# Performance work log

Hardware: AMD Instinct MI355X
Metric: run time of the kernel (lower is better)

The kernel has to match this reference:

```python
import jax, jax.numpy as jnp
import numpy as np

B, N, L = 512, 64, 64
D = 256          # item_embed_size / hidden_size
H = 256          # linear_hidden_size
V = 100000       # item_size
STEP = 1


def _p(key, shape, std=0.0625):
    return jax.random.uniform(key, shape, jnp.float32, -std, std)


def setup_inputs() -> dict:
    key = jax.random.key(0)
    ks = jax.random.split(key, 32)
    inp = {
        "alias_inputs": jax.random.randint(ks[0], (B, L), 0, N),
        "A": jax.random.uniform(ks[1], (B, N, 2 * N), jnp.float32),
        "items": jax.random.randint(ks[2], (B, N), 0, V),
        "mask": jnp.ones((B, L), jnp.int32),
        # parameters (stored as [in, out]; torch Linear applies x @ W.T + b)
        "emb": _p(ks[3], (V, D)),
        "W_ein": _p(ks[4], (D, D)), "b_ein": _p(ks[5], (D,)),
        "W_eout": _p(ks[6], (D, D)), "b_eout": _p(ks[7], (D,)),
        "b_iah": _p(ks[8], (D,)), "b_oah": _p(ks[9], (D,)),
        "W_i": _p(ks[10], (2 * D, 3 * D)), "b_i": _p(ks[11], (3 * D,)),
        "W_h": _p(ks[12], (D, 3 * D)), "b_h": _p(ks[13], (3 * D,)),
        "W1": _p(ks[14], (D, D)), "b1": _p(ks[15], (D,)),
        "W2": _p(ks[16], (D, D)), "b2": _p(ks[17], (D,)),
        "W3": _p(ks[18], (D, 1)),
        "Wn1": _p(ks[19], (2 * D, H)), "bn1": _p(ks[20], (H,)),
        "Wn2": _p(ks[21], (H, D)), "bn2": _p(ks[22], (D,)),
    }
    return inp


def reference(alias_inputs, A, items, mask,
              emb, W_ein, b_ein, W_eout, b_eout, b_iah, b_oah,
              W_i, b_i, W_h, b_h, W1, b1, W2, b2, W3, Wn1, bn1, Wn2, bn2):
    n = A.shape[1]
    hidden = emb[items]  # [B, N, D] (dropout is identity at eval)

    def gnn_cell(h):
        inp_in = jnp.matmul(A[:, :, :n], h @ W_ein + b_ein) + b_iah
        inp_out = jnp.matmul(A[:, :, n:2 * n], h @ W_eout + b_eout) + b_oah
        inputs = jnp.concatenate([inp_in, inp_out], axis=2)     # [B, N, 2D]
        gi = inputs @ W_i + b_i                                  # [B, N, 3D]
        gh = h @ W_h + b_h                                       # [B, N, 3D]
        i_r, i_i, i_n = jnp.split(gi, 3, axis=2)
        h_r, h_i, h_n = jnp.split(gh, 3, axis=2)
        resetgate = jax.nn.sigmoid(i_r + h_r)
        inputgate = jax.nn.sigmoid(i_i + h_i)
        newgate = jnp.tanh(i_n + resetgate * h_n)
        return newgate + inputgate * (h - newgate)

    for _ in range(STEP):
        hidden = gnn_cell(hidden)

    # per-sample gather of node states into sequence order
    seq_hidden = jnp.take_along_axis(hidden, alias_inputs[:, :, None], axis=1)  # [B, L, D]
    last = jnp.sum(mask, axis=1) - 1
    ht = seq_hidden[jnp.arange(seq_hidden.shape[0]), last]        # [B, D]

    q1 = (ht @ W1 + b1)[:, None, :]                               # [B, 1, D]
    q2 = seq_hidden @ W2 + b2                                     # [B, L, D]
    alpha = jax.nn.sigmoid(q1 + q2) @ W3                          # [B, L, 1]
    a = jnp.sum(alpha * seq_hidden * mask[:, :, None].astype(jnp.float32), axis=1)  # [B, D]

    x = jnp.concatenate([a, ht], axis=1)                          # [B, 2D]
    return jax.nn.relu(x @ Wn1 + bn1) @ Wn2 + bn2                 # [B, D]
```

## Files before the change

kernel.cpp:

```cpp
#include <hip/hip_runtime.h>
#include <hip/hip_bf16.h>
#include <math.h>

typedef short bhalf8 __attribute__((ext_vector_type(8)));
typedef float floatx4 __attribute__((ext_vector_type(4)));

__device__ __forceinline__ float sigmoidf_(float x) { return 1.0f / (1.0f + __expf(-x)); }

__device__ __forceinline__ unsigned short f2bf(float f) {
    unsigned int u = __builtin_bit_cast(unsigned int, f);
    u += 0x7FFFu + ((u >> 16) & 1u);
    return (unsigned short)(u >> 16);
}
__device__ __forceinline__ float bf2f(unsigned short h) {
    unsigned int u = ((unsigned int)h) << 16;
    return __builtin_bit_cast(float, u);
}

__device__ __forceinline__ floatx4 mfma16(bhalf8 a, bhalf8 b, floatx4 c) {
    return __builtin_amdgcn_mfma_f32_16x16x32_bf16(a, b, c, 0, 0, 0);
}

__device__ __forceinline__ void gl_lds16(const unsigned short* g, unsigned short* l) {
    __builtin_amdgcn_global_load_lds(
        (const __attribute__((address_space(1))) void*)g,
        (__attribute__((address_space(3))) void*)l, 16, 0, 0);
}

__device__ __forceinline__ void pack_generic(
    int b, int tid, const float* __restrict__ W0, const float* __restrict__ W1,
    int split, int N, int BN, unsigned short* __restrict__ out)
{
    int t = b * 256 + tid;
    int j = t & 7;
    int lane = (t >> 3) & 63;
    int FT = BN >> 4;
    int f = (t >> 9) % FT;
    int rest = t / (512 * FT);
    int NT = N / BN;
    int nt = rest % NT;
    int kt = rest / NT;
    int k = kt * 32 + (lane >> 4) * 8 + j;
    int n = nt * BN + f * 16 + (lane & 15);
    float v = (n < split) ? W0[(size_t)k * split + n]
                          : W1[(size_t)k * (N - split) + (n - split)];
    out[t] = f2bf(v);
}

__device__ __forceinline__ void pack_gru_(
    int b, int tid, const float* __restrict__ Wi, const float* __restrict__ Wh,
    unsigned short* __restrict__ out)
{
    int t = b * 256 + tid;
    int j = t & 7;
    int lane = (t >> 3) & 63;
    int f = (t >> 9) & 3;
    int q = t >> 11;
    int g = q % 3;
    int p = q / 3;
    int dt = p & 3;
    int kt = p >> 2;
    int k = kt * 32 + (lane >> 4) * 8 + j;
    int n = g * 256 + dt * 64 + f * 16 + (lane & 15);
    float v = (k < 512) ? Wi[(size_t)k * 768 + n] : Wh[(size_t)(k - 512) * 768 + n];
    out[t] = f2bf(v);
}

__global__ __launch_bounds__(256) void pack_all(
    const float* __restrict__ W_ein, const float* __restrict__ W_eout,
    const float* __restrict__ Wi, const float* __restrict__ Wh,
    const float* __restrict__ W2, const float* __restrict__ Wn1,
    const float* __restrict__ Wn2,
    unsigned short* __restrict__ Wio_pk, unsigned short* __restrict__ Wg_pk,
    unsigned short* __restrict__ W2pk, unsigned short* __restrict__ Wn1pk,
    unsigned short* __restrict__ Wn2pk)
{
    int bx = blockIdx.x;
    int tid = threadIdx.x;
    if (bx < 512)       pack_generic(bx,        tid, W_ein, W_eout, 256, 512, 128, Wio_pk);
    else if (bx < 2816) pack_gru_   (bx - 512,  tid, Wi, Wh, Wg_pk);
    else if (bx < 3072) pack_generic(bx - 2816, tid, W2,  W2,  256, 256, 256, W2pk);
    else if (bx < 3584) pack_generic(bx - 3072, tid, Wn1, Wn1, 256, 256, 256, Wn1pk);
    else                pack_generic(bx - 3584, tid, Wn2, Wn2, 256, 256, 256, Wn2pk);
}

__global__ __launch_bounds__(256) void gather_emb(
    const int* __restrict__ items, const float* __restrict__ emb,
    unsigned short* __restrict__ hidden_pk)
{
    int i = blockIdx.x * 256 + threadIdx.x;
    int mg = i >> 9;
    int rem = i & 511;
    int l = rem & 63;
    int m = mg * 16 + (l & 15);
    int k = (rem >> 6) * 32 + (l >> 4) * 8;
    int it = items[m];
    const float* src = emb + (size_t)it * 256 + k;
    float4 v0 = *(const float4*)src;
    float4 v1 = *(const float4*)(src + 4);
    uint4 o;
    o.x = f2bf(v0.x) | ((unsigned)f2bf(v0.y) << 16);
    o.y = f2bf(v0.z) | ((unsigned)f2bf(v0.w) << 16);
    o.z = f2bf(v1.x) | ((unsigned)f2bf(v1.y) << 16);
    o.w = f2bf(v1.z) | ((unsigned)f2bf(v1.w) << 16);
    *(uint4*)(hidden_pk + (size_t)i * 8) = o;
}

__global__ __launch_bounds__(256) void gemm_hio_mfma(
    const unsigned short* __restrict__ hidden_pk,
    const unsigned short* __restrict__ Wio_pk,
    const float* __restrict__ bein, const float* __restrict__ beout,
    unsigned short* __restrict__ hio_pk)
{
    __shared__ unsigned short As[2][4096];
    __shared__ unsigned short Bs[2][4096];
    const int tid = threadIdx.x;
    const int wid = tid >> 6, lane = tid & 63;
    const int wr = wid >> 1, wc = wid & 1;
    const int bm = blockIdx.x * 128;
    const int nt = blockIdx.y;
    const int mg0 = bm >> 4;

    auto stage = [&](int kt, int buf) {
        #pragma unroll
        for (int u = 0; u < 2; ++u) {
            int rg = wid * 2 + u;
            gl_lds16(hidden_pk + ((size_t)(mg0 + rg) * 8 + kt) * 512 + lane * 8, &As[buf][rg * 512]);
            gl_lds16(Wio_pk + ((size_t)(kt * 4 + nt) * 8 + rg) * 512 + lane * 8, &Bs[buf][rg * 512]);
        }
    };

    floatx4 acc[4][4] = {};
    stage(0, 0);
    __syncthreads();
    #pragma unroll
    for (int kt = 0; kt < 8; ++kt) {
        int cur = kt & 1;
        if (kt < 7) stage(kt + 1, cur ^ 1);
        bhalf8 a[4], b[4];
        #pragma unroll
        for (int i = 0; i < 4; i++) a[i] = *(const bhalf8*)&As[cur][(wr * 4 + i) * 512 + lane * 8];
        #pragma unroll
        for (int j = 0; j < 4; j++) b[j] = *(const bhalf8*)&Bs[cur][(wc * 4 + j) * 512 + lane * 8];
        #pragma unroll
        for (int i = 0; i < 4; i++)
            #pragma unroll
            for (int j = 0; j < 4; j++) acc[i][j] = mfma16(a[i], b[j], acc[i][j]);
        __syncthreads();
    }
    const int r0 = (lane >> 4) * 4;
    #pragma unroll
    for (int mf = 0; mf < 4; mf++) {
        int m0 = bm + wr * 64 + mf * 16 + r0;
        int b_ = m0 >> 6;
        int ml = m0 & 63;
        int ktb = ml >> 5;
        int k0 = ml & 31;
        int j0 = k0 & 7;
        #pragma unroll
        for (int nf = 0; nf < 4; nf++) {
            int ng = nt * 128 + wc * 64 + nf * 16 + (lane & 15);
            int half = ng >> 8;
            int nh = ng & 255;
            float bias = half ? beout[nh] : bein[nh];
            int lane_b = ((k0 >> 3) << 4) + (nh & 15);
            size_t pb = ((((size_t)(b_ * 2 + half) * 2 + ktb) * 16 + (nh >> 4)) * 64 + lane_b) * 8 + j0;
            ushort4 o;
            o.x = f2bf(acc[mf][nf][0] + bias);
            o.y = f2bf(acc[mf][nf][1] + bias);
            o.z = f2bf(acc[mf][nf][2] + bias);
            o.w = f2bf(acc[mf][nf][3] + bias);
            *(ushort4*)(hio_pk + pb) = o;
        }
    }
}

__global__ __launch_bounds__(256) void adj_mfma(
    const float* __restrict__ A,
    const unsigned short* __restrict__ hio_pk,
    const float* __restrict__ biah, const float* __restrict__ boah,
    unsigned short* __restrict__ inp_pk)
{
    __shared__ unsigned short As_[2048];
    __shared__ unsigned short Bs_[8192];
    const int b = blockIdx.x;
    const int half = blockIdx.y;
    const int tid = threadIdx.x;
    const int wid = tid >> 6, lane = tid & 63;

    floatx4 acc[4][4] = {};
    #pragma unroll
    for (int kt = 0; kt < 2; ++kt) {
        {
            int r = tid >> 2, jj = tid & 3;
            const float* src = A + (size_t)b * 8192 + r * 128 + half * 64 + kt * 32 + jj * 8;
            float4 v0 = *(const float4*)src;
            float4 v1 = *(const float4*)(src + 4);
            uint4 o;
            o.x = f2bf(v0.x) | ((unsigned)f2bf(v0.y) << 16);
            o.y = f2bf(v0.z) | ((unsigned)f2bf(v0.w) << 16);
            o.z = f2bf(v1.x) | ((unsigned)f2bf(v1.y) << 16);
            o.w = f2bf(v1.z) | ((unsigned)f2bf(v1.w) << 16);
            *(uint4*)&As_[((r >> 4) * 64 + jj * 16 + (r & 15)) * 8] = o;
        }
        {
            const unsigned short* src = hio_pk + (size_t)((b * 2 + half) * 2 + kt) * 8192;
            #pragma unroll
            for (int u = 0; u < 4; ++u) {
                int sg = wid * 4 + u;
                gl_lds16(src + sg * 512 + lane * 8, &Bs_[sg * 512]);
            }
        }
        __syncthreads();
        bhalf8 a[4], bb[4];
        #pragma unroll
        for (int i = 0; i < 4; i++) a[i] = *(const bhalf8*)&As_[(i * 64 + lane) * 8];
        #pragma unroll
        for (int j = 0; j < 4; j++) bb[j] = *(const bhalf8*)&Bs_[((wid * 4 + j) * 64 + lane) * 8];
        #pragma unroll
        for (int i = 0; i < 4; i++)
            #pragma unroll
            for (int j = 0; j < 4; j++) acc[i][j] = mfma16(a[i], bb[j], acc[i][j]);
        __syncthreads();
    }
    const float* bias = half ? boah : biah;
    const int r0 = (lane >> 4) * 4;
    #pragma unroll
    for (int i = 0; i < 4; i++) {
        #pragma unroll
        for (int j = 0; j < 4; j++) {
            int nh = wid * 64 + j * 16 + (lane & 15);
            float bv = bias[nh];
            int kt5 = half * 8 + wid * 2 + (j >> 1);
            int l2 = ((j & 1) * 2 + ((lane >> 3) & 1)) * 16;
            #pragma unroll
            for (int reg = 0; reg < 4; reg++) {
                int mlo = r0 + reg;
                size_t dst = (((size_t)(b * 4 + i) * 16 + kt5) * 64 + l2 + mlo) * 8 + (lane & 7);
                inp_pk[dst] = f2bf(acc[i][j][reg] + bv);
            }
        }
    }
}

__global__ __launch_bounds__(256) void gru_mfma(
    const unsigned short* __restrict__ inp_pk,
    const unsigned short* __restrict__ hidden_pk,
    const unsigned short* __restrict__ Wg_pk,
    const float* __restrict__ bi, const float* __restrict__ bh,
    unsigned short* __restrict__ newh_bf)
{
    __shared__ unsigned short As3[3][4096];
    __shared__ unsigned short Bs2[2][6144];
    const int tid = threadIdx.x;
    const int wid = tid >> 6, lane = tid & 63;
    const int wr = wid >> 1, wc = wid & 1;
    const int bm = blockIdx.x * 128;
    const int dt = blockIdx.y;
    const int mg0 = bm >> 4;

    floatx4 R[4][2] = {}, I[4][2] = {}, N0[4][2] = {}, N1[4][2] = {};

    auto stageA = [&](int st, int buf) {
        #pragma unroll
        for (int u = 0; u < 2; ++u) {
            int rg = wid * 2 + u;
            const unsigned short* src = (st < 16)
                ? inp_pk    + ((size_t)(mg0 + rg) * 16 + st) * 512
                : hidden_pk + ((size_t)(mg0 + rg) * 8 + (st - 16)) * 512;
            gl_lds16(src + lane * 8, &As3[buf][rg * 512]);
        }
    };
    auto stageB = [&](int st, int buf) {
        #pragma unroll
        for (int u = 0; u < 3; ++u) {
            int sg = wid * 3 + u;
            gl_lds16(Wg_pk + ((size_t)(st * 4 + dt) * 12 + sg) * 512 + lane * 8,
                     &Bs2[buf][sg * 512]);
        }
    };

    stageA(0, 0);
    stageB(0, 0);
    stageA(1, 1);
    #pragma unroll
    for (int st = 0; st < 24; ++st) {
        const int ca = st % 3, cb = st & 1;
        if (st < 23) asm volatile("s_waitcnt vmcnt(2)" ::: "memory");
        else         asm volatile("s_waitcnt vmcnt(0)" ::: "memory");
        __builtin_amdgcn_s_barrier();
        __builtin_amdgcn_sched_barrier(0);
        if (st < 23) stageB(st + 1, cb ^ 1);
        if (st < 22) stageA(st + 2, (st + 2) % 3);
        bhalf8 a[4];
        #pragma unroll
        for (int i = 0; i < 4; i++)
            a[i] = *(const bhalf8*)&As3[ca][(wr * 4 + i) * 512 + lane * 8];
        #pragma unroll
        for (int f = 0; f < 2; ++f) {
            bhalf8 bv = *(const bhalf8*)&Bs2[cb][(0 * 4 + wc * 2 + f) * 512 + lane * 8];
            #pragma unroll
            for (int i = 0; i < 4; i++) R[i][f] = mfma16(a[i], bv, R[i][f]);
        }
        #pragma unroll
        for (int f = 0; f < 2; ++f) {
            bhalf8 bv = *(const bhalf8*)&Bs2[cb][(1 * 4 + wc * 2 + f) * 512 + lane * 8];
            #pragma unroll
            for (int i = 0; i < 4; i++) I[i][f] = mfma16(a[i], bv, I[i][f]);
        }
        if (st < 16) {
            #pragma unroll
            for (int f = 0; f < 2; ++f) {
                bhalf8 bv = *(const bhalf8*)&Bs2[cb][(2 * 4 + wc * 2 + f) * 512 + lane * 8];
                #pragma unroll
                for (int i = 0; i < 4; i++) N0[i][f] = mfma16(a[i], bv, N0[i][f]);
            }
        } else {
            #pragma unroll
            for (int f = 0; f < 2; ++f) {
                bhalf8 bv = *(const bhalf8*)&Bs2[cb][(2 * 4 + wc * 2 + f) * 512 + lane * 8];
                #pragma unroll
                for (int i = 0; i < 4; i++) N1[i][f] = mfma16(a[i], bv, N1[i][f]);
            }
        }
    }
    const int r0 = (lane >> 4) * 4;
    const int bd = dt * 64 + wc * 32;
    #pragma unroll
    for (int i = 0; i < 4; i++) {
        #pragma unroll
        for (int f = 0; f < 2; f++) {
            int d = bd + f * 16 + (lane & 15);
            float bir = bi[d] + bh[d];
            float bii = bi[256 + d] + bh[256 + d];
            float bin = bi[512 + d];
            float bhn = bh[512 + d];
            #pragma unroll
            for (int reg = 0; reg < 4; reg++) {
                int m = bm + wr * 64 + i * 16 + r0 + reg;
                size_t hidx = (((size_t)(m >> 4) * 8 + (d >> 5)) * 64
                               + ((d >> 3) & 3) * 16 + (m & 15)) * 8 + (d & 7);
                float hv = bf2f(hidden_pk[hidx]);
                float rg = sigmoidf_(R[i][f][reg] + bir);
                float ig = sigmoidf_(I[i][f][reg] + bii);
                float ng = tanhf(N0[i][f][reg] + bin + rg * (N1[i][f][reg] + bhn));
                newh_bf[(size_t)m * 256 + d] = f2bf(ng + ig * (hv - ng));
            }
        }
    }
}

__global__ __launch_bounds__(256) void attn_fused(
    const unsigned short* __restrict__ newh_bf,
    const int* __restrict__ alias, const int* __restrict__ mask,
    const float* __restrict__ W1, const float* __restrict__ b1,
    const float* __restrict__ b2, const float* __restrict__ W3,
    const unsigned short* __restrict__ W2pk,
    unsigned short* __restrict__ ht_bf,
    unsigned short* __restrict__ a_bf)
{
    const int b = blockIdx.x;
    const int tid = threadIdx.x;
    const int wid = tid >> 6, lane = tid & 63;
    __shared__ int arow[64];
    __shared__ int node_s;
    __shared__ float hts[256];
    __shared__ float q1s[256];
    __shared__ float alphap[4][64];
    __shared__ float am[64];
    __shared__ unsigned short As[2048];
    __shared__ unsigned short Bs[8192];
    if (tid < 64) {
        arow[tid] = b * 64 + alias[b * 64 + tid];
        int mv = mask[b * 64 + tid];
        #pragma unroll
        for (int off = 32; off > 0; off >>= 1) mv += __shfl_xor(mv, off);
        if (tid == 0) node_s = b * 64 + alias[b * 64 + (mv - 1)];
    }
    __syncthreads();
    {
        unsigned short hv = newh_bf[(size_t)node_s * 256 + tid];
        ht_bf[(size_t)b * 256 + tid] = hv;
        hts[tid] = bf2f(hv);
    }
    __syncthreads();
    {
        float q0 = 0, q1v = 0, q2v = 0, q3v = 0;
        for (int k = 0; k < 256; k += 4) {
            q0  = fmaf(hts[k],     W1[(size_t)k * 256 + tid],       q0);
            q1v = fmaf(hts[k + 1], W1[(size_t)(k + 1) * 256 + tid], q1v);
            q2v = fmaf(hts[k + 2], W1[(size_t)(k + 2) * 256 + tid], q2v);
            q3v = fmaf(hts[k + 3], W1[(size_t)(k + 3) * 256 + tid], q3v);
        }
        q1s[tid] = (q0 + q1v) + (q2v + q3v) + b1[tid];
    }

    floatx4 acc[4][4] = {};
    #pragma unroll
    for (int kt = 0; kt < 8; ++kt) {
        {
            int r = tid >> 2, jj = tid & 3;
            const unsigned short* src = newh_bf + (size_t)arow[r] * 256 + kt * 32 + jj * 8;
            *(uint4*)&As[((r >> 4) * 64 + jj * 16 + (r & 15)) * 8] = *(const uint4*)src;
        }
        {
            const unsigned short* src = W2pk + (size_t)kt * 16 * 512;
            #pragma unroll
            for (int u = 0; u < 4; ++u) {
                int sg = wid * 4 + u;
                gl_lds16(src + sg * 512 + lane * 8, &Bs[sg * 512]);
            }
        }
        __syncthreads();
        bhalf8 a[4], bb[4];
        #pragma unroll
        for (int i = 0; i < 4; i++) a[i] = *(const bhalf8*)&As[(i * 64 + lane) * 8];
        #pragma unroll
        for (int j = 0; j < 4; j++) bb[j] = *(const bhalf8*)&Bs[((wid * 4 + j) * 64 + lane) * 8];
        #pragma unroll
        for (int i = 0; i < 4; i++)
            #pragma unroll
            for (int j = 0; j < 4; j++) acc[i][j] = mfma16(a[i], bb[j], acc[i][j]);
        __syncthreads();
    }
    float q1v[4], b2v[4], w3v[4];
    #pragma unroll
    for (int j = 0; j < 4; j++) {
        int col = wid * 64 + j * 16 + (lane & 15);
        q1v[j] = q1s[col];
        b2v[j] = b2[col];
        w3v[j] = W3[col];
    }
    #pragma unroll
    for (int i = 0; i < 4; i++) {
        #pragma unroll
        for (int reg = 0; reg < 4; reg++) {
            float t = 0.f;
            #pragma unroll
            for (int j = 0; j < 4; j++)
                t += sigmoidf_(acc[i][j][reg] + q1v[j] + b2v[j]) * w3v[j];
            #pragma unroll
            for (int off = 1; off < 16; off <<= 1) t += __shfl_xor(t, off);
            if ((lane & 15) == 0) alphap[wid][i * 16 + (lane >> 4) * 4 + reg] = t;
        }
    }
    __syncthreads();
    if (tid < 64) {
        float al = alphap[0][tid] + alphap[1][tid] + alphap[2][tid] + alphap[3][tid];
        am[tid] = al * (float)mask[b * 64 + tid];
    }
    __syncthreads();
    float acca = 0.f;
    #pragma unroll 8
    for (int l = 0; l < 64; ++l)
        acca = fmaf(am[l], bf2f(newh_bf[(size_t)arow[l] * 256 + tid]), acca);
    a_bf[(size_t)b * 256 + tid] = f2bf(acca);
}

__global__ __launch_bounds__(256) void mlp_fused(
    const unsigned short* __restrict__ a_bf, const unsigned short* __restrict__ ht_bf,
    const unsigned short* __restrict__ Wn1pk, const float* __restrict__ bn1,
    const unsigned short* __restrict__ Wn2pk, const float* __restrict__ bn2,
    float* __restrict__ out)
{
    __shared__ unsigned short As[4096];
    __shared__ unsigned short Bs[16384];
    __shared__ unsigned short Ys[16384];
    const int tid = threadIdx.x;
    const int wid = tid >> 6, lane = tid & 63;
    const int bm = blockIdx.x * 64;
    const int c = lane & 15;
    const int r0 = (lane >> 4) * 4;

    {
        floatx4 acc[4][4] = {};
        #pragma unroll
        for (int s = 0; s < 8; ++s) {
            #pragma unroll
            for (int v = 0; v < 2; ++v) {
                int kt = s * 2 + v;
                int r = tid >> 2, jj = tid & 3;
                const unsigned short* src = ((kt < 8) ? a_bf : ht_bf)
                    + (size_t)(bm + r) * 256 + (kt & 7) * 32 + jj * 8;
                *(uint4*)&As[v * 2048 + ((r >> 4) * 64 + jj * 16 + (r & 15)) * 8] = *(const uint4*)src;
            }
            #pragma unroll
            for (int u = 0; u < 8; ++u) {
                int sg = wid * 8 + u;
                int ktl = sg >> 4, f = sg & 15;
                gl_lds16(Wn1pk + ((size_t)(s * 2 + ktl) * 16 + f) * 512 + lane * 8, &Bs[sg * 512]);
            }
            __syncthreads();
            #pragma unroll
            for (int v = 0; v < 2; ++v) {
                bhalf8 a[4], bb[4];
                #pragma unroll
                for (int i = 0; i < 4; i++) a[i] = *(const bhalf8*)&As[v * 2048 + (i * 64 + lane) * 8];
                #pragma unroll
                for (int j = 0; j < 4; j++) bb[j] = *(const bhalf8*)&Bs[((v * 16) + wid * 4 + j) * 512 + lane * 8];
                #pragma unroll
                for (int i = 0; i < 4; i++)
                    #pragma unroll
                    for (int j = 0; j < 4; j++) acc[i][j] = mfma16(a[i], bb[j], acc[i][j]);
            }
            __syncthreads();
        }
        #pragma unroll
        for (int i = 0; i < 4; i++) {
            #pragma unroll
            for (int jf = 0; jf < 4; jf++) {
                int n = wid * 64 + jf * 16 + c;
                float bv = bn1[n];
                int kt2 = wid * 2 + (jf >> 1);
                int l2 = ((jf & 1) * 2 + (c >> 3)) * 16;
                #pragma unroll
                for (int reg = 0; reg < 4; reg++) {
                    float v = fmaxf(acc[i][jf][reg] + bv, 0.f);
                    size_t idx = (((size_t)(kt2 * 4 + i) * 64) + l2 + r0 + reg) * 8 + (c & 7);
                    Ys[idx] = f2bf(v);
                }
            }
        }
    }
    __syncthreads();
    floatx4 acc2[4][4] = {};
    #pragma unroll
    for (int s = 0; s < 4; ++s) {
        #pragma unroll
        for (int u = 0; u < 8; ++u) {
            int sg = wid * 8 + u;
            int ktl = sg >> 4, f = sg & 15;
            gl_lds16(Wn2pk + ((size_t)(s * 2 + ktl) * 16 + f) * 512 + lane * 8, &Bs[sg * 512]);
        }
        __syncthreads();
        #pragma unroll
        for (int v = 0; v < 2; ++v) {
            int kt2 = s * 2 + v;
            bhalf8 a[4], bb[4];
            #pragma unroll
            for (int i = 0; i < 4; i++) a[i] = *(const bhalf8*)&Ys[((kt2 * 4 + i) * 64 + lane) * 8];
            #pragma unroll
            for (int j = 0; j < 4; j++) bb[j] = *(const bhalf8*)&Bs[((v * 16) + wid * 4 + j) * 512 + lane * 8];
            #pragma unroll
            for (int i = 0; i < 4; i++)
                #pragma unroll
                for (int j = 0; j < 4; j++) acc2[i][j] = mfma16(a[i], bb[j], acc2[i][j]);
        }
        __syncthreads();
    }
    #pragma unroll
    for (int i = 0; i < 4; i++) {
        #pragma unroll
        for (int jf = 0; jf < 4; jf++) {
            int n = wid * 64 + jf * 16 + c;
            float bv = bn2[n];
            #pragma unroll
            for (int reg = 0; reg < 4; reg++) {
                int m = bm + i * 16 + r0 + reg;
                out[(size_t)m * 256 + n] = acc2[i][jf][reg] + bv;
            }
        }
    }
}

extern "C" void kernel_launch(void* const* d_in, const int* in_sizes, int n_in,
                              void* d_out, int out_size, void* d_ws, size_t ws_size,
                              hipStream_t stream)
{
    const int*   alias  = (const int*)  d_in[0];
    const float* A      = (const float*)d_in[1];
    const int*   items  = (const int*)  d_in[2];
    const int*   mask   = (const int*)  d_in[3];
    const float* emb    = (const float*)d_in[4];
    const float* W_ein  = (const float*)d_in[5];
    const float* b_ein  = (const float*)d_in[6];
    const float* W_eout = (const float*)d_in[7];
    const float* b_eout = (const float*)d_in[8];
    const float* b_iah  = (const float*)d_in[9];
    const float* b_oah  = (const float*)d_in[10];
    const float* W_i    = (const float*)d_in[11];
    const float* b_i    = (const float*)d_in[12];
    const float* W_h    = (const float*)d_in[13];
    const float* b_h    = (const float*)d_in[14];
    const float* W1     = (const float*)d_in[15];
    const float* b1     = (const float*)d_in[16];
    const float* W2     = (const float*)d_in[17];
    const float* b2     = (const float*)d_in[18];
    const float* W3     = (const float*)d_in[19];
    const float* Wn1    = (const float*)d_in[20];
    const float* bn1    = (const float*)d_in[21];
    const float* Wn2    = (const float*)d_in[22];
    const float* bn2    = (const float*)d_in[23];
    float* out = (float*)d_out;
    (void)in_sizes; (void)n_in; (void)out_size; (void)ws_size;

    char* w = (char*)d_ws;
    unsigned short* hidden_pk = (unsigned short*)(w);
    unsigned short* hio_pk    = (unsigned short*)(w + 16777216);
    unsigned short* inp_pk    = (unsigned short*)(w + 50331648);
    unsigned short* newh_bf   = (unsigned short*)(w + 83886080);
    unsigned short* Wio_pk    = (unsigned short*)(w + 100663296);
    unsigned short* Wg_pk     = (unsigned short*)(w + 100925440);
    unsigned short* W2pk      = (unsigned short*)(w + 102105088);
    unsigned short* Wn1pk     = (unsigned short*)(w + 102236160);
    unsigned short* Wn2pk     = (unsigned short*)(w + 102498304);
    unsigned short* ht_bf     = (unsigned short*)(w + 102629376);
    unsigned short* a_bf      = (unsigned short*)(w + 102891520);

    pack_all<<<3840, 256, 0, stream>>>(W_ein, W_eout, W_i, W_h, W2, Wn1, Wn2,
                                       Wio_pk, Wg_pk, W2pk, Wn1pk, Wn2pk);
    gather_emb   <<<4096, 256, 0, stream>>>(items, emb, hidden_pk);
    gemm_hio_mfma<<<dim3(256, 4), 256, 0, stream>>>(hidden_pk, Wio_pk, b_ein, b_eout, hio_pk);
    adj_mfma     <<<dim3(512, 2), 256, 0, stream>>>(A, hio_pk, b_iah, b_oah, inp_pk);
    gru_mfma     <<<dim3(256, 4), 256, 0, stream>>>(inp_pk, hidden_pk, Wg_pk, b_i, b_h, newh_bf);
    attn_fused   <<<512, 256, 0, stream>>>(newh_bf, alias, mask, W1, b1, b2, W3, W2pk, ht_bf, a_bf);
    mlp_fused    <<<8, 256, 0, stream>>>(a_bf, ht_bf, Wn1pk, bn1, Wn2pk, bn2, out);
}
```

Baseline: 153.5 us.

## Fuse edge-projection GEMM with adjacency matmul through shared memory

Merges the hidden@W_ein/W_eout GEMM and the adjacency batched matmul into one kernel. The projected tile (two samples by 128 columns) is written into LDS in MFMA B-operand layout. It is then multiplied by the bf16-converted A slices for those samples, so the hio intermediate never goes to global memory and one launch is dropped. In exchange, each block now reads the A slices for its half, which duplicates A reads across the two column tiles, and it uses more LDS per block.

```diff
diff --git a/kernel.cpp b/kernel.cpp
--- a/kernel.cpp
+++ b/kernel.cpp
@@ -106,27 +106,37 @@
     *(uint4*)(hidden_pk + (size_t)i * 8) = o;
 }
 
-__global__ __launch_bounds__(256) void gemm_hio_mfma(
+__global__ __launch_bounds__(256) void gemm_hioadj(
     const unsigned short* __restrict__ hidden_pk,
     const unsigned short* __restrict__ Wio_pk,
     const float* __restrict__ bein, const float* __restrict__ beout,
-    unsigned short* __restrict__ hio_pk)
-{
-    __shared__ unsigned short As[2][4096];
-    __shared__ unsigned short Bs[2][4096];
+    const float* __restrict__ A,
+    const float* __restrict__ biah, const float* __restrict__ boah,
+    unsigned short* __restrict__ inp_pk)
+{
+    __shared__ unsigned short SM[24576];
+    unsigned short* As0 = SM;
+    unsigned short* Bs0 = SM + 8192;
+    unsigned short* Hb  = SM;
+    unsigned short* Ab  = SM + 16384;
+
     const int tid = threadIdx.x;
     const int wid = tid >> 6, lane = tid & 63;
     const int wr = wid >> 1, wc = wid & 1;
     const int bm = blockIdx.x * 128;
     const int nt = blockIdx.y;
     const int mg0 = bm >> 4;
+    const int b0 = blockIdx.x * 2;
+    const int half = nt >> 1;
 
     auto stage = [&](int kt, int buf) {
         #pragma unroll
         for (int u = 0; u < 2; ++u) {
             int rg = wid * 2 + u;
-            gl_lds16(hidden_pk + ((size_t)(mg0 + rg) * 8 + kt) * 512 + lane * 8, &As[buf][rg * 512]);
-            gl_lds16(Wio_pk + ((size_t)(kt * 4 + nt) * 8 + rg) * 512 + lane * 8, &Bs[buf][rg * 512]);
+            gl_lds16(hidden_pk + ((size_t)(mg0 + rg) * 8 + kt) * 512 + lane * 8,
+                     &As0[buf * 4096 + rg * 512]);
+            gl_lds16(Wio_pk + ((size_t)(kt * 4 + nt) * 8 + rg) * 512 + lane * 8,
+                     &Bs0[buf * 4096 + rg * 512]);
         }
     };
 
@@ -139,9 +149,9 @@
         if (kt < 7) stage(kt + 1, cur ^ 1);
         bhalf8 a[4], b[4];
         #pragma unroll
-        for (int i = 0; i < 4; i++) a[i] = *(const bhalf8*)&As[cur][(wr * 4 + i) * 512 + lane * 8];
-        #pragma unroll
-        for (int j = 0; j < 4; j++) b[j] = *(const bhalf8*)&Bs[cur][(wc * 4 + j) * 512 + lane * 8];
+        for (int i = 0; i < 4; i++) a[i] = *(const bhalf8*)&As0[cur * 4096 + (wr * 4 + i) * 512 + lane * 8];
+        #pragma unroll
+        for (int j = 0; j < 4; j++) b[j] = *(const bhalf8*)&Bs0[cur * 4096 + (wc * 4 + j) * 512 + lane * 8];
         #pragma unroll
         for (int i = 0; i < 4; i++)
             #pragma unroll
@@ -149,95 +159,75 @@
         __syncthreads();
     }
     const int r0 = (lane >> 4) * 4;
-    #pragma unroll
-    for (int mf = 0; mf < 4; mf++) {
-        int m0 = bm + wr * 64 + mf * 16 + r0;
-        int b_ = m0 >> 6;
-        int ml = m0 & 63;
-        int ktb = ml >> 5;
-        int k0 = ml & 31;
-        int j0 = k0 & 7;
-        #pragma unroll
-        for (int nf = 0; nf < 4; nf++) {
-            int ng = nt * 128 + wc * 64 + nf * 16 + (lane & 15);
-            int half = ng >> 8;
-            int nh = ng & 255;
-            float bias = half ? beout[nh] : bein[nh];
-            int lane_b = ((k0 >> 3) << 4) + (nh & 15);
-            size_t pb = ((((size_t)(b_ * 2 + half) * 2 + ktb) * 16 + (nh >> 4)) * 64 + lane_b) * 8 + j0;
-            ushort4 o;
-            o.x = f2bf(acc[mf][nf][0] + bias);
-            o.y = f2bf(acc[mf][nf][1] + bias);
-            o.z = f2bf(acc[mf][nf][2] + bias);
-            o.w = f2bf(acc[mf][nf][3] + bias);
-            *(ushort4*)(hio_pk + pb) = o;
-        }
-    }
-}
-
-__global__ __launch_bounds__(256) void adj_mfma(
-    const float* __restrict__ A,
-    const unsigned short* __restrict__ hio_pk,
-    const float* __restrict__ biah, const float* __restrict__ boah,
-    unsigned short* __restrict__ inp_pk)
-{
-    __shared__ unsigned short As_[2048];
-    __shared__ unsigned short Bs_[8192];
-    const int b = blockIdx.x;
-    const int half = blockIdx.y;
-    const int tid = threadIdx.x;
-    const int wid = tid >> 6, lane = tid & 63;
-
-    floatx4 acc[4][4] = {};
-    #pragma unroll
-    for (int kt = 0; kt < 2; ++kt) {
-        {
-            int r = tid >> 2, jj = tid & 3;
-            const float* src = A + (size_t)b * 8192 + r * 128 + half * 64 + kt * 32 + jj * 8;
-            float4 v0 = *(const float4*)src;
-            float4 v1 = *(const float4*)(src + 4);
-            uint4 o;
-            o.x = f2bf(v0.x) | ((unsigned)f2bf(v0.y) << 16);
-            o.y = f2bf(v0.z) | ((unsigned)f2bf(v0.w) << 16);
-            o.z = f2bf(v1.x) | ((unsigned)f2bf(v1.y) << 16);
-            o.w = f2bf(v1.z) | ((unsigned)f2bf(v1.w) << 16);
-            *(uint4*)&As_[((r >> 4) * 64 + jj * 16 + (r & 15)) * 8] = o;
-        }
-        {
-            const unsigned short* src = hio_pk + (size_t)((b * 2 + half) * 2 + kt) * 8192;
-            #pragma unroll
-            for (int u = 0; u < 4; ++u) {
-                int sg = wid * 4 + u;
-                gl_lds16(src + sg * 512 + lane * 8, &Bs_[sg * 512]);
-            }
-        }
-        __syncthreads();
-        bhalf8 a[4], bb[4];
-        #pragma unroll
-        for (int i = 0; i < 4; i++) a[i] = *(const bhalf8*)&As_[(i * 64 + lane) * 8];
-        #pragma unroll
-        for (int j = 0; j < 4; j++) bb[j] = *(const bhalf8*)&Bs_[((wid * 4 + j) * 64 + lane) * 8];
+    {
+        const float* bio = half ? beout : bein;
+        #pragma unroll
+        for (int mf = 0; mf < 4; mf++) {
+            #pragma unroll
+            for (int nf = 0; nf < 4; nf++) {
+                int nl = wc * 64 + nf * 16 + (lane & 15);
+                float bias = bio[(nt & 1) * 128 + nl];
+                int base = (((wr * 2 + (mf >> 1)) * 8 + (nl >> 4)) * 64
+                            + ((mf & 1) * 2 + (r0 >> 3)) * 16 + (lane & 15)) * 8 + (r0 & 7);
+                ushort4 o;
+                o.x = f2bf(acc[mf][nf][0] + bias);
+                o.y = f2bf(acc[mf][nf][1] + bias);
+                o.z = f2bf(acc[mf][nf][2] + bias);
+                o.w = f2bf(acc[mf][nf][3] + bias);
+                *(ushort4*)&Hb[base] = o;
+            }
+        }
+    }
+    {
+        int r = tid >> 2, jj = tid & 3;
+        #pragma unroll
+        for (int bb = 0; bb < 2; ++bb)
+            #pragma unroll
+            for (int kt2 = 0; kt2 < 2; ++kt2) {
+                const float* src = A + (size_t)(b0 + bb) * 8192 + r * 128 + half * 64 + kt2 * 32 + jj * 8;
+                float4 v0 = *(const float4*)src;
+                float4 v1 = *(const float4*)(src + 4);
+                uint4 o;
+                o.x = f2bf(v0.x) | ((unsigned)f2bf(v0.y) << 16);
+                o.y = f2bf(v0.z) | ((unsigned)f2bf(v0.w) << 16);
+                o.z = f2bf(v1.x) | ((unsigned)f2bf(v1.y) << 16);
+                o.w = f2bf(v1.z) | ((unsigned)f2bf(v1.w) << 16);
+                *(uint4*)&Ab[(bb * 2 + kt2) * 2048 + ((r >> 4) * 64 + jj * 16 + (r & 15)) * 8] = o;
+            }
+    }
+    __syncthreads();
+    const int bb = wid >> 1, ch = wid & 1;
+    floatx4 acc2[4][4] = {};
+    #pragma unroll
+    for (int kt2 = 0; kt2 < 2; ++kt2) {
+        bhalf8 a2[4];
         #pragma unroll
         for (int i = 0; i < 4; i++)
-            #pragma unroll
-            for (int j = 0; j < 4; j++) acc[i][j] = mfma16(a[i], bb[j], acc[i][j]);
-        __syncthreads();
-    }
-    const float* bias = half ? boah : biah;
-    const int r0 = (lane >> 4) * 4;
-    #pragma unroll
-    for (int i = 0; i < 4; i++) {
-        #pragma unroll
-        for (int j = 0; j < 4; j++) {
-            int nh = wid * 64 + j * 16 + (lane & 15);
-            float bv = bias[nh];
-            int kt5 = half * 8 + wid * 2 + (j >> 1);
-            int l2 = ((j & 1) * 2 + ((lane >> 3) & 1)) * 16;
-            #pragma unroll
-            for (int reg = 0; reg < 4; reg++) {
-                int mlo = r0 + reg;
-                size_t dst = (((size_t)(b * 4 + i) * 16 + kt5) * 64 + l2 + mlo) * 8 + (lane & 7);
-                inp_pk[dst] = f2bf(acc[i][j][reg] + bv);
+            a2[i] = *(const bhalf8*)&Ab[(bb * 2 + kt2) * 2048 + (i * 64 + lane) * 8];
+        #pragma unroll
+        for (int jf = 0; jf < 4; jf++) {
+            bhalf8 bv = *(const bhalf8*)&Hb[((bb * 2 + kt2) * 8 + ch * 4 + jf) * 512 + lane * 8];
+            #pragma unroll
+            for (int i = 0; i < 4; i++) acc2[i][jf] = mfma16(a2[i], bv, acc2[i][jf]);
+        }
+    }
+    {
+        const float* bia = half ? boah : biah;
+        const int b = b0 + bb;
+        #pragma unroll
+        for (int i = 0; i < 4; i++) {
+            #pragma unroll
+            for (int jf = 0; jf < 4; jf++) {
+                int colp = (nt & 1) * 128 + (ch * 4 + jf) * 16 + (lane & 15);
+                float bv = bia[colp];
+                int kt5 = nt * 4 + ch * 2 + (jf >> 1);
+                int l2 = ((jf & 1) * 2 + ((lane >> 3) & 1)) * 16;
+                #pragma unroll
+                for (int reg = 0; reg < 4; reg++) {
+                    int mlo = r0 + reg;
+                    size_t dst = (((size_t)(b * 4 + i) * 16 + kt5) * 64 + l2 + mlo) * 8 + (lane & 7);
+                    inp_pk[dst] = f2bf(acc2[i][jf][reg] + bv);
+                }
             }
         }
     }
@@ -596,7 +586,6 @@
 
     char* w = (char*)d_ws;
     unsigned short* hidden_pk = (unsigned short*)(w);
-    unsigned short* hio_pk    = (unsigned short*)(w + 16777216);
     unsigned short* inp_pk    = (unsigned short*)(w + 50331648);
     unsigned short* newh_bf   = (unsigned short*)(w + 83886080);
     unsigned short* Wio_pk    = (unsigned short*)(w + 100663296);
@@ -609,10 +598,10 @@
 
     pack_all<<<3840, 256, 0, stream>>>(W_ein, W_eout, W_i, W_h, W2, Wn1, Wn2,
                                        Wio_pk, Wg_pk, W2pk, Wn1pk, Wn2pk);
-    gather_emb   <<<4096, 256, 0, stream>>>(items, emb, hidden_pk);
-    gemm_hio_mfma<<<dim3(256, 4), 256, 0, stream>>>(hidden_pk, Wio_pk, b_ein, b_eout, hio_pk);
-    adj_mfma     <<<dim3(512, 2), 256, 0, stream>>>(A, hio_pk, b_iah, b_oah, inp_pk);
-    gru_mfma     <<<dim3(256, 4), 256, 0, stream>>>(inp_pk, hidden_pk, Wg_pk, b_i, b_h, newh_bf);
-    attn_fused   <<<512, 256, 0, stream>>>(newh_bf, alias, mask, W1, b1, b2, W3, W2pk, ht_bf, a_bf);
-    mlp_fused    <<<8, 256, 0, stream>>>(a_bf, ht_bf, Wn1pk, bn1, Wn2pk, bn2, out);
-}
+    gather_emb <<<4096, 256, 0, stream>>>(items, emb, hidden_pk);
+    gemm_hioadj<<<dim3(256, 4), 256, 0, stream>>>(hidden_pk, Wio_pk, b_ein, b_eout,
+                                                  A, b_iah, b_oah, inp_pk);
+    gru_mfma   <<<dim3(256, 4), 256, 0, stream>>>(inp_pk, hidden_pk, Wg_pk, b_i, b_h, newh_bf);
+    attn_fused <<<512, 256, 0, stream>>>(newh_bf, alias, mask, W1, b1, b2, W3, W2pk, ht_bf, a_bf);
+    mlp_fused  <<<8, 256, 0, stream>>>(a_bf, ht_bf, Wn1pk, bn1, Wn2pk, bn2, out);
+}
```

New measurement: 140.4 us. 8.5% less time.
